# Performance work log

Hardware: AMD Instinct MI355X
Metric: run time of the kernel (lower is better)

The kernel has to match this reference:

```python
import jax, jax.numpy as jnp
import numpy as np

D_GAUSS = 5
N_GAUSS = 100
IN_DIM = 768
T = 100000
LN_EPS = 1e-5


def setup_inputs() -> dict:
    key = jax.random.key(0)
    kx, kw, kb, kc = jax.random.split(key, 4)
    x = jax.random.normal(kx, (T, IN_DIM), dtype=jnp.float32)
    # nn.Linear(input_dim, gaussian_dim)
    lim = 1.0 / np.sqrt(IN_DIM)
    W = jax.random.uniform(kw, (D_GAUSS, IN_DIM), minval=-lim, maxval=lim, dtype=jnp.float32)
    b = jax.random.uniform(kb, (D_GAUSS,), minval=-lim, maxval=lim, dtype=jnp.float32)
    # GM centers (random init, as in GMLayer)
    centers = jax.random.normal(kc, (N_GAUSS, D_GAUSS), dtype=jnp.float32)
    # covariance init exactly as in Gaussian_Layer.__init__: isotropic,
    # scale = (mean nearest-neighbor center distance / 2)^2
    c_np = np.asarray(centers, dtype=np.float64)
    dist = np.sqrt(((c_np[:, None, :] - c_np[None, :, :]) ** 2).sum(-1))
    np.fill_diagonal(dist, np.inf)
    scale = (dist.min(axis=1).mean() / 2.0) ** 2
    cov = np.broadcast_to(np.eye(D_GAUSS) * scale, (N_GAUSS, D_GAUSS, D_GAUSS)).copy()
    covariance = jnp.asarray(cov, dtype=jnp.float32)
    gamma = jnp.ones((N_GAUSS,), dtype=jnp.float32)
    beta = jnp.zeros((N_GAUSS,), dtype=jnp.float32)
    return {"x": x, "W": W, "b": b, "centers": centers,
            "covariance": covariance, "gamma": gamma, "beta": beta}


def reference(x, W, b, centers, covariance, gamma, beta):
    # Linear + Sigmoid projection: [T, d]
    z = jax.nn.sigmoid(x @ W.T + b)
    # Gaussian mixture likelihood per gaussian: [T, K]
    inv_cov = jnp.linalg.inv(covariance)                      # [K, d, d]
    sign, logdet = jnp.linalg.slogdet(covariance)             # [K]
    diff = z[:, None, :] - centers[None, :, :]                # [T, K, d]
    maha = jnp.einsum('tki,kij,tkj->tk', diff, inv_cov, diff)  # [T, K]
    d = centers.shape[-1]
    log2pi = jnp.log(jnp.asarray(2.0 * np.pi, dtype=z.dtype))
    lik = jnp.exp(-0.5 * (maha + d * log2pi + logdet[None, :]))  # [T, K]
    # LayerNorm over the n_gaussians axis
    mu = lik.mean(axis=-1, keepdims=True)
    var = jnp.mean((lik - mu) ** 2, axis=-1, keepdims=True)
    normed = (lik - mu) * jax.lax.rsqrt(var + LN_EPS) * gamma + beta
    # MeanLayer over instances, then squeeze(0): output [K]
    return normed.mean(axis=0)
```

## Files before the change

### kernel.cpp

```cpp
#include <hip/hip_runtime.h>
#include <math.h>

#define D_G 5
#define N_G 100
#define IN_DIM 768
#define T_ROWS 100000
#define LN_EPS 1e-5f

__global__ void precompute_gauss(const float* __restrict__ cov,
                                 float* __restrict__ coeffs) {
    int k = blockIdx.x * blockDim.x + threadIdx.x;
    if (k >= N_G) return;
    double a[D_G][D_G], inv[D_G][D_G];
    for (int i = 0; i < D_G; ++i)
        for (int j = 0; j < D_G; ++j) {
            a[i][j] = (double)cov[(k * D_G + i) * D_G + j];
            inv[i][j] = (i == j) ? 1.0 : 0.0;
        }
    double det = 1.0;
    for (int c = 0; c < D_G; ++c) {
        int p = c;
        double best = fabs(a[c][c]);
        for (int r = c + 1; r < D_G; ++r) {
            double v = fabs(a[r][c]);
            if (v > best) { best = v; p = r; }
        }
        if (p != c) {
            for (int j = 0; j < D_G; ++j) {
                double t = a[c][j]; a[c][j] = a[p][j]; a[p][j] = t;
                t = inv[c][j]; inv[c][j] = inv[p][j]; inv[p][j] = t;
            }
            det = -det;
        }
        double piv = a[c][c];
        det *= piv;
        double ip = 1.0 / piv;
        for (int j = 0; j < D_G; ++j) { a[c][j] *= ip; inv[c][j] *= ip; }
        for (int r = 0; r < D_G; ++r) {
            if (r == c) continue;
            double f = a[r][c];
            if (f != 0.0)
                for (int j = 0; j < D_G; ++j) {
                    a[r][j] -= f * a[c][j];
                    inv[r][j] -= f * inv[c][j];
                }
        }
    }
    double logdet = log(fabs(det));
    float* o = coeffs + k * 16;
    for (int i = 0; i < D_G; ++i) o[i] = (float)inv[i][i];
    int idx = D_G;
    for (int i = 0; i < D_G; ++i)
        for (int j = i + 1; j < D_G; ++j) o[idx++] = (float)(2.0 * inv[i][j]);
    o[15] = (float)(-0.5 * ((double)D_G * log(2.0 * 3.14159265358979323846) + logdet));
}

__device__ __forceinline__ float gm_eval(const float z[D_G], const float* ct,
                                         const float* cf, float cc) {
    float d0 = z[0] - ct[0];
    float d1 = z[1] - ct[1];
    float d2 = z[2] - ct[2];
    float d3 = z[3] - ct[3];
    float d4 = z[4] - ct[4];
    float m = cf[0] * (d0 * d0);
    m = fmaf(cf[1], d1 * d1, m);
    m = fmaf(cf[2], d2 * d2, m);
    m = fmaf(cf[3], d3 * d3, m);
    m = fmaf(cf[4], d4 * d4, m);
    m = fmaf(cf[5], d0 * d1, m);
    m = fmaf(cf[6], d0 * d2, m);
    m = fmaf(cf[7], d0 * d3, m);
    m = fmaf(cf[8], d0 * d4, m);
    m = fmaf(cf[9], d1 * d2, m);
    m = fmaf(cf[10], d1 * d3, m);
    m = fmaf(cf[11], d1 * d4, m);
    m = fmaf(cf[12], d2 * d3, m);
    m = fmaf(cf[13], d2 * d4, m);
    m = fmaf(cf[14], d3 * d4, m);
    return __expf(fmaf(-0.5f, m, cc));
}

__launch_bounds__(256)
__global__ void gm_main(const float* __restrict__ x, const float* __restrict__ W,
                        const float* __restrict__ bb,
                        const float* __restrict__ centers,
                        const float* __restrict__ coeffs,
                        float* __restrict__ partials, int nblk) {
    const int lane = threadIdx.x & 63;
    const int wid = threadIdx.x >> 6;
    const int gw = blockIdx.x * 4 + wid;
    const int nw = nblk * 4;

    float4 wreg[D_G][3];
#pragma unroll
    for (int j = 0; j < D_G; ++j)
#pragma unroll
        for (int i = 0; i < 3; ++i)
            wreg[j][i] = *reinterpret_cast<const float4*>(W + j * IN_DIM + i * 256 + lane * 4);

    float bj[D_G];
#pragma unroll
    for (int j = 0; j < D_G; ++j) bj[j] = bb[j];

    const int k0 = lane;
    const bool has1 = lane < (N_G - 64);
    const int k1 = has1 ? (64 + lane) : lane;

    float cf0[15], cf1[15], ct0[D_G], ct1[D_G];
#pragma unroll
    for (int i = 0; i < 15; ++i) { cf0[i] = coeffs[k0 * 16 + i]; cf1[i] = coeffs[k1 * 16 + i]; }
#pragma unroll
    for (int i = 0; i < D_G; ++i) { ct0[i] = centers[k0 * D_G + i]; ct1[i] = centers[k1 * D_G + i]; }
    const float cc0 = coeffs[k0 * 16 + 15], cc1 = coeffs[k1 * 16 + 15];

    float acc0 = 0.f, acc1 = 0.f, accA = 0.f;

    int t = gw;
    float4 a0{}, a1{}, a2{};
    if (t < T_ROWS) {
        const float* xr = x + (size_t)t * IN_DIM + lane * 4;
        a0 = *reinterpret_cast<const float4*>(xr);
        a1 = *reinterpret_cast<const float4*>(xr + 256);
        a2 = *reinterpret_cast<const float4*>(xr + 512);
    }

    while (t < T_ROWS) {
        const int tn = t + nw;
        float4 b0{}, b1{}, b2{};
        if (tn < T_ROWS) {
            const float* xr = x + (size_t)tn * IN_DIM + lane * 4;
            b0 = *reinterpret_cast<const float4*>(xr);
            b1 = *reinterpret_cast<const float4*>(xr + 256);
            b2 = *reinterpret_cast<const float4*>(xr + 512);
        }

        float p[D_G];
#pragma unroll
        for (int j = 0; j < D_G; ++j) {
            const float4 w0 = wreg[j][0], w1 = wreg[j][1], w2 = wreg[j][2];
            float s = a0.x * w0.x;
            s = fmaf(a0.y, w0.y, s);
            s = fmaf(a0.z, w0.z, s);
            s = fmaf(a0.w, w0.w, s);
            s = fmaf(a1.x, w1.x, s);
            s = fmaf(a1.y, w1.y, s);
            s = fmaf(a1.z, w1.z, s);
            s = fmaf(a1.w, w1.w, s);
            s = fmaf(a2.x, w2.x, s);
            s = fmaf(a2.y, w2.y, s);
            s = fmaf(a2.z, w2.z, s);
            s = fmaf(a2.w, w2.w, s);
            p[j] = s;
        }
#pragma unroll
        for (int j = 0; j < D_G; ++j) {
#pragma unroll
            for (int m = 32; m >= 1; m >>= 1) p[j] += __shfl_xor(p[j], m, 64);
        }
        float z[D_G];
#pragma unroll
        for (int j = 0; j < D_G; ++j)
            z[j] = 1.0f / (1.0f + __expf(-(p[j] + bj[j])));

        const float lik0 = gm_eval(z, ct0, cf0, cc0);
        const float lik1 = has1 ? gm_eval(z, ct1, cf1, cc1) : 0.f;

        float s = lik0 + lik1;
        float q = fmaf(lik0, lik0, lik1 * lik1);
#pragma unroll
        for (int m = 32; m >= 1; m >>= 1) {
            s += __shfl_xor(s, m, 64);
            q += __shfl_xor(q, m, 64);
        }
        const float mu = s * (1.0f / N_G);
        float var = fmaf(q, 1.0f / N_G, -mu * mu);
        var = fmaxf(var, 0.f);
        const float r = rsqrtf(var + LN_EPS);
        acc0 = fmaf(lik0, r, acc0);
        if (has1) acc1 = fmaf(lik1, r, acc1);
        accA = fmaf(mu, r, accA);

        a0 = b0; a1 = b1; a2 = b2;
        t = tn;
    }

    __shared__ float sacc[N_G + 1];
    if (threadIdx.x < N_G + 1) sacc[threadIdx.x] = 0.f;
    __syncthreads();
    atomicAdd(&sacc[k0], acc0);
    if (has1) atomicAdd(&sacc[k1], acc1);
    if (lane == 0) atomicAdd(&sacc[N_G], accA);
    __syncthreads();
    if (threadIdx.x < N_G + 1)
        partials[(size_t)threadIdx.x * nblk + blockIdx.x] = sacc[threadIdx.x];
}

__global__ void reduce_partials(const float* __restrict__ partials,
                                const float* __restrict__ gamma_,
                                const float* __restrict__ beta_,
                                float* __restrict__ out, int nblk) {
    const int k = blockIdx.x;
    const int lane = threadIdx.x & 63;
    const int wid = threadIdx.x >> 6;
    double dk = 0.0, dA = 0.0;
    for (int b = threadIdx.x; b < nblk; b += blockDim.x) {
        dk += (double)partials[(size_t)k * nblk + b];
        dA += (double)partials[(size_t)N_G * nblk + b];
    }
#pragma unroll
    for (int m = 32; m >= 1; m >>= 1) {
        dk += __shfl_xor(dk, m, 64);
        dA += __shfl_xor(dA, m, 64);
    }
    __shared__ double sk[4], sA[4];
    if (lane == 0) { sk[wid] = dk; sA[wid] = dA; }
    __syncthreads();
    if (threadIdx.x == 0) {
        double S = sk[0] + sk[1] + sk[2] + sk[3];
        double A = sA[0] + sA[1] + sA[2] + sA[3];
        out[k] = (float)((double)gamma_[k] * (S - A) * (1.0 / (double)T_ROWS)
                         + (double)beta_[k]);
    }
}

extern "C" void kernel_launch(void* const* d_in, const int* in_sizes, int n_in,
                              void* d_out, int out_size, void* d_ws, size_t ws_size,
                              hipStream_t stream) {
    const float* x = (const float*)d_in[0];
    const float* W = (const float*)d_in[1];
    const float* b = (const float*)d_in[2];
    const float* centers = (const float*)d_in[3];
    const float* cov = (const float*)d_in[4];
    const float* gamma_ = (const float*)d_in[5];
    const float* beta_ = (const float*)d_in[6];
    float* out = (float*)d_out;

    float* ws = (float*)d_ws;
    float* coeffs = ws;
    float* partials = ws + N_G * 16;

    int nblk = 1024;
    {
        long avail = (long)(ws_size / sizeof(float)) - (long)(N_G * 16);
        long maxblk = avail / (N_G + 1);
        if (maxblk < nblk) nblk = (int)maxblk;
        if (nblk < 1) nblk = 1;
    }

    precompute_gauss<<<1, 128, 0, stream>>>(cov, coeffs);
    gm_main<<<nblk, 256, 0, stream>>>(x, W, b, centers, coeffs, partials, nblk);
    reduce_partials<<<N_G, 256, 0, stream>>>(partials, gamma_, beta_, out, nblk);
}
```

Measured before the change: 438.8 us.

## Process two rows per wavefront iteration to interleave reductions and loads

Each wavefront now handles a pair of adjacent rows per loop iteration. The two rows' dot products, shuffle reductions and Gaussian evaluations are interleaved to expose more instruction-level parallelism and to double the bytes in flight per prefetch. The sigmoid uses a hardware reciprocal, and the block count is halved with a launch-bounds occupancy hint. Register pressure rises from the doubled prefetch buffers, and the code assumes an even row count.

```diff
diff --git a/kernel.cpp b/kernel.cpp
--- a/kernel.cpp
+++ b/kernel.cpp
@@ -5,6 +5,7 @@
 #define N_G 100
 #define IN_DIM 768
 #define T_ROWS 100000
+#define N_PAIRS (T_ROWS / 2)
 #define LN_EPS 1e-5f
 
 __global__ void precompute_gauss(const float* __restrict__ cov,
@@ -80,7 +81,25 @@
     return __expf(fmaf(-0.5f, m, cc));
 }
 
-__launch_bounds__(256)
+__device__ __forceinline__ float dot12(const float4& xa, const float4& xb,
+                                       const float4& xc, const float4& w0,
+                                       const float4& w1, const float4& w2) {
+    float s = xa.x * w0.x;
+    s = fmaf(xa.y, w0.y, s);
+    s = fmaf(xa.z, w0.z, s);
+    s = fmaf(xa.w, w0.w, s);
+    s = fmaf(xb.x, w1.x, s);
+    s = fmaf(xb.y, w1.y, s);
+    s = fmaf(xb.z, w1.z, s);
+    s = fmaf(xb.w, w1.w, s);
+    s = fmaf(xc.x, w2.x, s);
+    s = fmaf(xc.y, w2.y, s);
+    s = fmaf(xc.z, w2.z, s);
+    s = fmaf(xc.w, w2.w, s);
+    return s;
+}
+
+__launch_bounds__(256, 2)
 __global__ void gm_main(const float* __restrict__ x, const float* __restrict__ W,
                         const float* __restrict__ bb,
                         const float* __restrict__ centers,
@@ -115,73 +134,86 @@
 
     float acc0 = 0.f, acc1 = 0.f, accA = 0.f;
 
-    int t = gw;
-    float4 a0{}, a1{}, a2{};
-    if (t < T_ROWS) {
-        const float* xr = x + (size_t)t * IN_DIM + lane * 4;
-        a0 = *reinterpret_cast<const float4*>(xr);
-        a1 = *reinterpret_cast<const float4*>(xr + 256);
-        a2 = *reinterpret_cast<const float4*>(xr + 512);
-    }
-
-    while (t < T_ROWS) {
-        const int tn = t + nw;
-        float4 b0{}, b1{}, b2{};
-        if (tn < T_ROWS) {
-            const float* xr = x + (size_t)tn * IN_DIM + lane * 4;
-            b0 = *reinterpret_cast<const float4*>(xr);
-            b1 = *reinterpret_cast<const float4*>(xr + 256);
-            b2 = *reinterpret_cast<const float4*>(xr + 512);
-        }
-
-        float p[D_G];
+    int pr = gw;
+    float4 A0{}, A1{}, A2{}, C0{}, C1{}, C2{};
+    if (pr < N_PAIRS) {
+        const float* xr = x + (size_t)(2 * pr) * IN_DIM + lane * 4;
+        A0 = *reinterpret_cast<const float4*>(xr);
+        A1 = *reinterpret_cast<const float4*>(xr + 256);
+        A2 = *reinterpret_cast<const float4*>(xr + 512);
+        C0 = *reinterpret_cast<const float4*>(xr + 768);
+        C1 = *reinterpret_cast<const float4*>(xr + 1024);
+        C2 = *reinterpret_cast<const float4*>(xr + 1280);
+    }
+
+    while (pr < N_PAIRS) {
+        const int pn = pr + nw;
+        float4 B0{}, B1{}, B2{}, D0{}, D1{}, D2{};
+        if (pn < N_PAIRS) {
+            const float* xr = x + (size_t)(2 * pn) * IN_DIM + lane * 4;
+            B0 = *reinterpret_cast<const float4*>(xr);
+            B1 = *reinterpret_cast<const float4*>(xr + 256);
+            B2 = *reinterpret_cast<const float4*>(xr + 512);
+            D0 = *reinterpret_cast<const float4*>(xr + 768);
+            D1 = *reinterpret_cast<const float4*>(xr + 1024);
+            D2 = *reinterpret_cast<const float4*>(xr + 1280);
+        }
+
+        float pA[D_G], pB[D_G];
 #pragma unroll
         for (int j = 0; j < D_G; ++j) {
-            const float4 w0 = wreg[j][0], w1 = wreg[j][1], w2 = wreg[j][2];
-            float s = a0.x * w0.x;
-            s = fmaf(a0.y, w0.y, s);
-            s = fmaf(a0.z, w0.z, s);
-            s = fmaf(a0.w, w0.w, s);
-            s = fmaf(a1.x, w1.x, s);
-            s = fmaf(a1.y, w1.y, s);
-            s = fmaf(a1.z, w1.z, s);
-            s = fmaf(a1.w, w1.w, s);
-            s = fmaf(a2.x, w2.x, s);
-            s = fmaf(a2.y, w2.y, s);
-            s = fmaf(a2.z, w2.z, s);
-            s = fmaf(a2.w, w2.w, s);
-            p[j] = s;
-        }
+            pA[j] = dot12(A0, A1, A2, wreg[j][0], wreg[j][1], wreg[j][2]);
+            pB[j] = dot12(C0, C1, C2, wreg[j][0], wreg[j][1], wreg[j][2]);
+        }
+#pragma unroll
+        for (int m = 32; m >= 1; m >>= 1) {
+#pragma unroll
+            for (int j = 0; j < D_G; ++j) {
+                pA[j] += __shfl_xor(pA[j], m, 64);
+                pB[j] += __shfl_xor(pB[j], m, 64);
+            }
+        }
+        float zA[D_G], zB[D_G];
 #pragma unroll
         for (int j = 0; j < D_G; ++j) {
-#pragma unroll
-            for (int m = 32; m >= 1; m >>= 1) p[j] += __shfl_xor(p[j], m, 64);
-        }
-        float z[D_G];
-#pragma unroll
-        for (int j = 0; j < D_G; ++j)
-            z[j] = 1.0f / (1.0f + __expf(-(p[j] + bj[j])));
-
-        const float lik0 = gm_eval(z, ct0, cf0, cc0);
-        const float lik1 = has1 ? gm_eval(z, ct1, cf1, cc1) : 0.f;
-
-        float s = lik0 + lik1;
-        float q = fmaf(lik0, lik0, lik1 * lik1);
+            zA[j] = __builtin_amdgcn_rcpf(1.0f + __expf(-(pA[j] + bj[j])));
+            zB[j] = __builtin_amdgcn_rcpf(1.0f + __expf(-(pB[j] + bj[j])));
+        }
+
+        const float likA0 = gm_eval(zA, ct0, cf0, cc0);
+        const float eA1 = gm_eval(zA, ct1, cf1, cc1);
+        const float likA1 = has1 ? eA1 : 0.f;
+        const float likB0 = gm_eval(zB, ct0, cf0, cc0);
+        const float eB1 = gm_eval(zB, ct1, cf1, cc1);
+        const float likB1 = has1 ? eB1 : 0.f;
+
+        float sA = likA0 + likA1;
+        float qA = fmaf(likA0, likA0, likA1 * likA1);
+        float sB = likB0 + likB1;
+        float qB = fmaf(likB0, likB0, likB1 * likB1);
 #pragma unroll
         for (int m = 32; m >= 1; m >>= 1) {
-            s += __shfl_xor(s, m, 64);
-            q += __shfl_xor(q, m, 64);
-        }
-        const float mu = s * (1.0f / N_G);
-        float var = fmaf(q, 1.0f / N_G, -mu * mu);
-        var = fmaxf(var, 0.f);
-        const float r = rsqrtf(var + LN_EPS);
-        acc0 = fmaf(lik0, r, acc0);
-        if (has1) acc1 = fmaf(lik1, r, acc1);
-        accA = fmaf(mu, r, accA);
-
-        a0 = b0; a1 = b1; a2 = b2;
-        t = tn;
+            sA += __shfl_xor(sA, m, 64);
+            qA += __shfl_xor(qA, m, 64);
+            sB += __shfl_xor(sB, m, 64);
+            qB += __shfl_xor(qB, m, 64);
+        }
+        const float muA = sA * (1.0f / N_G);
+        float varA = fmaf(qA, 1.0f / N_G, -muA * muA);
+        varA = fmaxf(varA, 0.f);
+        const float rA = rsqrtf(varA + LN_EPS);
+        const float muB = sB * (1.0f / N_G);
+        float varB = fmaf(qB, 1.0f / N_G, -muB * muB);
+        varB = fmaxf(varB, 0.f);
+        const float rB = rsqrtf(varB + LN_EPS);
+
+        acc0 = fmaf(likA0, rA, fmaf(likB0, rB, acc0));
+        acc1 = fmaf(likA1, rA, fmaf(likB1, rB, acc1));
+        accA = fmaf(muA, rA, fmaf(muB, rB, accA));
+
+        A0 = B0; A1 = B1; A2 = B2;
+        C0 = D0; C1 = D1; C2 = D2;
+        pr = pn;
     }
 
     __shared__ float sacc[N_G + 1];
@@ -239,7 +271,7 @@
     float* coeffs = ws;
     float* partials = ws + N_G * 16;
 
-    int nblk = 1024;
+    int nblk = 512;
     {
         long avail = (long)(ws_size / sizeof(float)) - (long)(N_G * 16);
         long maxblk = avail / (N_G + 1);
```

After: 434.2 us. Within noise of the previous version (-1.0%).
